# Optimization experiments

Hardware: AMD Instinct MI355X
Metric: run time of the kernel (lower is better)

Reference implementation:

```python
import jax, jax.numpy as jnp
import numpy as np

N_NODES = 100000
N_EDGES = 3200000
IN_CH = 32
HID = 64
OUT_CH = 2


def _sage_conv(x, src, tgt, W_l, W_r, b, n_nodes):
    """PyG SAGEConv with mean aggregation: out = lin_l(mean_agg) + lin_r(x).
    edge (src -> tgt): messages from src nodes are averaged at tgt nodes."""
    msgs = x[src]  # [E, C] gather
    agg = jax.ops.segment_sum(msgs, tgt, num_segments=n_nodes)  # [N, C]
    deg = jax.ops.segment_sum(jnp.ones((src.shape[0],), x.dtype), tgt,
                              num_segments=n_nodes)  # [N]
    agg = agg / jnp.maximum(deg, 1.0)[:, None]
    return agg @ W_l + b + x @ W_r


def _layernorm(x, gamma, beta, eps=1e-5):
    mu = jnp.mean(x, axis=-1, keepdims=True)
    var = jnp.var(x, axis=-1, keepdims=True)
    return (x - mu) * jax.lax.rsqrt(var + eps) * gamma + beta


def setup_inputs() -> dict:
    key = jax.random.key(0)
    ks = jax.random.split(key, 12)
    x = jax.random.normal(ks[0], (N_NODES, IN_CH), dtype=jnp.float32)
    edge_index = jax.random.randint(ks[1], (2, N_EDGES), 0, N_NODES, dtype=jnp.int64)

    def lin(k, fan_in, fan_out):
        s = 1.0 / np.sqrt(fan_in)
        return jax.random.uniform(k, (fan_in, fan_out), jnp.float32, -s, s)

    return {
        "x": x,
        "edge_index": edge_index,
        "W_l1": lin(ks[2], IN_CH, HID), "W_r1": lin(ks[3], IN_CH, HID),
        "b1": jnp.zeros((HID,), jnp.float32),
        "g1": jnp.ones((HID,), jnp.float32), "be1": jnp.zeros((HID,), jnp.float32),
        "W_l2": lin(ks[4], HID, HID), "W_r2": lin(ks[5], HID, HID),
        "b2": jnp.zeros((HID,), jnp.float32),
        "g2": jnp.ones((HID,), jnp.float32), "be2": jnp.zeros((HID,), jnp.float32),
        "W_l3": lin(ks[6], HID, OUT_CH), "W_r3": lin(ks[7], HID, OUT_CH),
        "b3": jnp.zeros((OUT_CH,), jnp.float32),
    }


def reference(x, edge_index, W_l1, W_r1, b1, g1, be1,
              W_l2, W_r2, b2, g2, be2, W_l3, W_r3, b3):
    src = edge_index[0]
    tgt = edge_index[1]
    n = x.shape[0]
    # layer 1: SAGEConv -> LayerNorm -> ReLU (dropout = identity in eval)
    h = _sage_conv(x, src, tgt, W_l1, W_r1, b1, n)
    h = jax.nn.relu(_layernorm(h, g1, be1))
    # layer 2
    h = _sage_conv(h, src, tgt, W_l2, W_r2, b2, n)
    h = jax.nn.relu(_layernorm(h, g2, be2))
    # layer 3 -> logits [N, OUT_CH]
    logits = _sage_conv(h, src, tgt, W_l3, W_r3, b3, n)
    return logits
```

## Files before the change

kernel.cpp:

```cpp
#include <hip/hip_runtime.h>
#include <hip/hip_fp16.h>

#define N_NODES 100000
#define N_EDGES 3200000
#define NBK 391
#define CAP 9216
#define EPB 8192
#define NBLK_BIN 391


__device__ __forceinline__ int wave_incl_scan_i(int v) {
  int lane = threadIdx.x & 63;
#pragma unroll
  for (int off = 1; off < 64; off <<= 1) {
    int n = __shfl_up(v, off);
    if (lane >= off) v += n;
  }
  return v;
}

__device__ __forceinline__ float bcastf(float v, int l) {
  return __int_as_float(__builtin_amdgcn_readlane(__float_as_int(v), l));
}

__device__ __forceinline__ __half2 h2zero() { return __float2half2_rn(0.0f); }

__device__ __forceinline__ __half2 h2shfl_xor_add(__half2 a, int off) {
  int ai = *reinterpret_cast<int*>(&a);
  int bi = __shfl_xor(ai, off);
  return __hadd2(a, *reinterpret_cast<__half2*>(&bi));
}


__global__ __launch_bounds__(256) void init_cursor(int* __restrict__ cursor) {
  int i = blockIdx.x * 256 + threadIdx.x;
  if (i < NBK) cursor[i] = i * CAP;
}

__global__ __launch_bounds__(256) void bin_scatter(const int* __restrict__ src,
                                                   const int* __restrict__ tgt,
                                                   int* __restrict__ cursor,
                                                   unsigned int* __restrict__ binned) {
  __shared__ int hist[NBK];
  __shared__ int lbase[NBK];
  int t = threadIdx.x;
  for (int i = t; i < NBK; i += 256) hist[i] = 0;
  __syncthreads();
  int e0 = blockIdx.x * EPB;
  int e1 = min(e0 + EPB, N_EDGES);
  for (int e = e0 + t; e < e1; e += 256) atomicAdd(&hist[tgt[e] >> 8], 1);
  __syncthreads();
  for (int i = t; i < NBK; i += 256) {
    int c = hist[i];
    lbase[i] = c ? atomicAdd(&cursor[i], c) : 0;
    hist[i] = 0;
  }
  __syncthreads();
  for (int e = e0 + t; e < e1; e += 256) {
    int tg = tgt[e];
    int bkt = tg >> 8;
    int lo = atomicAdd(&hist[bkt], 1);
    binned[lbase[bkt] + lo] = (unsigned int)src[e] | ((unsigned int)(tg & 255) << 17);
  }
}

__global__ __launch_bounds__(256) void bucket_sort(const unsigned int* __restrict__ binned,
                                                   const int* __restrict__ cursor,
                                                   int* __restrict__ csr,
                                                   int* __restrict__ offs) {
  __shared__ int deg[256];
  __shared__ int lcur[256];
  __shared__ int wsum[4];
  int b = blockIdx.x;
  int t = threadIdx.x;
  int base = b * CAP;
  int cnt = cursor[b] - base;
  deg[t] = 0;
  __syncthreads();
  for (int i = t; i < cnt; i += 256) atomicAdd(&deg[binned[base + i] >> 17], 1);
  __syncthreads();
  int v = deg[t];
  int inc = wave_incl_scan_i(v);
  int lane = t & 63, wid = t >> 6;
  if (lane == 63) wsum[wid] = inc;
  __syncthreads();
  if (t == 0) {
    int run = 0;
#pragma unroll
    for (int i = 0; i < 4; i++) { int c = wsum[i]; wsum[i] = run; run += c; }
  }
  __syncthreads();
  int incl = inc + wsum[wid];
  lcur[t] = base + incl - v;
  int node = b * 256 + t;
  if (node < N_NODES) offs[node] = base + incl;
  __syncthreads();
  for (int i = t; i < cnt; i += 256) {
    unsigned int pv = binned[base + i];
    int pos = atomicAdd(&lcur[pv >> 17], 1);
    csr[pos] = (int)(pv & 0x1FFFFu);
  }
}


__global__ __launch_bounds__(256) void to_half2(const float* __restrict__ in,
                                                __half2* __restrict__ out, int n2) {
  int i = blockIdx.x * 256 + threadIdx.x;
  if (i >= n2) return;
  float2 v = reinterpret_cast<const float2*>(in)[i];
  out[i] = __floats2half2_rn(v.x, v.y);
}


__global__ __launch_bounds__(256) void layer1_fused(
    const __half2* __restrict__ xh, const int* __restrict__ csr,
    const int* __restrict__ offs, const float* __restrict__ Wl,
    const float* __restrict__ Wr, const float* __restrict__ b,
    const float* __restrict__ g, const float* __restrict__ be,
    __half* __restrict__ h1) {
  int node = blockIdx.x * 4 + (threadIdx.x >> 6);
  if (node >= N_NODES) return;
  int lane = threadIdx.x & 63;
  int c = lane & 15, slot4 = lane >> 4;

  int end = offs[node];
  int start = (node & 255) ? offs[node - 1] : (node >> 8) * CAP;
  float inv = 1.0f / fmaxf((float)(end - start), 1.0f);

  __half2 A0 = h2zero(), A1 = h2zero(), A2 = h2zero(), A3 = h2zero();
  int slot = start + slot4;
  for (; slot + 12 < end; slot += 16) {
    int s0 = csr[slot], s1 = csr[slot + 4], s2 = csr[slot + 8], s3 = csr[slot + 12];
    A0 = __hadd2(A0, xh[(size_t)s0 * 16 + c]);
    A1 = __hadd2(A1, xh[(size_t)s1 * 16 + c]);
    A2 = __hadd2(A2, xh[(size_t)s2 * 16 + c]);
    A3 = __hadd2(A3, xh[(size_t)s3 * 16 + c]);
  }
  if (slot < end) {
    int i1 = slot + 4, i2 = slot + 8;
    int s0 = csr[slot];
    int s1 = (i1 < end) ? csr[i1] : s0;
    int s2 = (i2 < end) ? csr[i2] : s0;
    __half2 u0 = xh[(size_t)s0 * 16 + c];
    __half2 u1 = xh[(size_t)s1 * 16 + c];
    __half2 u2 = xh[(size_t)s2 * 16 + c];
    A0 = __hadd2(A0, u0);
    A1 = __hadd2(A1, (i1 < end) ? u1 : h2zero());
    A2 = __hadd2(A2, (i2 < end) ? u2 : h2zero());
  }
  __half2 Ah = __hadd2(__hadd2(A0, A1), __hadd2(A2, A3));
  Ah = h2shfl_xor_add(Ah, 16);
  Ah = h2shfl_xor_add(Ah, 32);
  float2 fa = __half22float2(Ah);
  float ax = fa.x * inv, ay = fa.y * inv;

  float2 xs = __half22float2(xh[(size_t)node * 16 + c]);

  int o = lane;
  float accO = b[o];
#pragma unroll
  for (int k = 0; k < 32; k++) {
    float ak = bcastf((k & 1) ? ay : ax, k >> 1);
    float xk = bcastf((k & 1) ? xs.y : xs.x, k >> 1);
    accO = fmaf(ak, Wl[k * 64 + o], accO);
    accO = fmaf(xk, Wr[k * 64 + o], accO);
  }

  float s = accO;
#pragma unroll
  for (int off = 32; off; off >>= 1) s += __shfl_xor(s, off);
  float mu = s * (1.0f / 64.0f);
  float d = accO - mu;
  float v2 = d * d;
#pragma unroll
  for (int off = 32; off; off >>= 1) v2 += __shfl_xor(v2, off);
  float o2 = d * rsqrtf(v2 * (1.0f / 64.0f) + 1e-5f) * g[o] + be[o];
  h1[(size_t)node * 64 + o] = __float2half(fmaxf(o2, 0.0f));
}

__global__ __launch_bounds__(256) void layer2_fused(
    const __half2* __restrict__ h1q, const int* __restrict__ csr,
    const int* __restrict__ offs, const float* __restrict__ Wl,
    const float* __restrict__ Wr, const float* __restrict__ b,
    const float* __restrict__ g, const float* __restrict__ be,
    const float* __restrict__ Wl3, const float* __restrict__ Wr3,
    const float* __restrict__ b3, float* __restrict__ y3,
    float* __restrict__ out) {
  int node = blockIdx.x * 4 + (threadIdx.x >> 6);
  if (node >= N_NODES) return;
  int lane = threadIdx.x & 63;
  int c = lane & 31, half = lane >> 5;

  int end = offs[node];
  int start = (node & 255) ? offs[node - 1] : (node >> 8) * CAP;
  float inv = 1.0f / fmaxf((float)(end - start), 1.0f);

  __half2 A0 = h2zero(), A1 = h2zero(), A2 = h2zero(), A3 = h2zero();
  int slot = start + half;
  for (; slot + 6 < end; slot += 8) {
    int s0 = csr[slot], s1 = csr[slot + 2], s2 = csr[slot + 4], s3 = csr[slot + 6];
    A0 = __hadd2(A0, h1q[(size_t)s0 * 32 + c]);
    A1 = __hadd2(A1, h1q[(size_t)s1 * 32 + c]);
    A2 = __hadd2(A2, h1q[(size_t)s2 * 32 + c]);
    A3 = __hadd2(A3, h1q[(size_t)s3 * 32 + c]);
  }
  if (slot < end) {
    int i1 = slot + 2, i2 = slot + 4;
    int s0 = csr[slot];
    int s1 = (i1 < end) ? csr[i1] : s0;
    int s2 = (i2 < end) ? csr[i2] : s0;
    __half2 u0 = h1q[(size_t)s0 * 32 + c];
    __half2 u1 = h1q[(size_t)s1 * 32 + c];
    __half2 u2 = h1q[(size_t)s2 * 32 + c];
    A0 = __hadd2(A0, u0);
    A1 = __hadd2(A1, (i1 < end) ? u1 : h2zero());
    A2 = __hadd2(A2, (i2 < end) ? u2 : h2zero());
  }
  __half2 Ah = __hadd2(__hadd2(A0, A1), __hadd2(A2, A3));
  Ah = h2shfl_xor_add(Ah, 32);
  float2 fa = __half22float2(Ah);
  float ax = fa.x * inv, ay = fa.y * inv;

  float2 hs = __half22float2(h1q[(size_t)node * 32 + c]);

  int o = lane;
  float accO = b[o];
#pragma unroll
  for (int k = 0; k < 64; k++) {
    float ak = bcastf((k & 1) ? ay : ax, k >> 1);
    float hk = bcastf((k & 1) ? hs.y : hs.x, k >> 1);
    accO = fmaf(ak, Wl[k * 64 + o], accO);
    accO = fmaf(hk, Wr[k * 64 + o], accO);
  }

  float s = accO;
#pragma unroll
  for (int off = 32; off; off >>= 1) s += __shfl_xor(s, off);
  float mu = s * (1.0f / 64.0f);
  float d = accO - mu;
  float v2 = d * d;
#pragma unroll
  for (int off = 32; off; off >>= 1) v2 += __shfl_xor(v2, off);
  float h2v = fmaxf(d * rsqrtf(v2 * (1.0f / 64.0f) + 1e-5f) * g[o] + be[o], 0.0f);

  float t0 = h2v * Wl3[o * 2 + 0];
  float t1 = h2v * Wl3[o * 2 + 1];
  float t2 = h2v * Wr3[o * 2 + 0];
  float t3 = h2v * Wr3[o * 2 + 1];
#pragma unroll
  for (int off = 32; off; off >>= 1) {
    t0 += __shfl_xor(t0, off);
    t1 += __shfl_xor(t1, off);
    t2 += __shfl_xor(t2, off);
    t3 += __shfl_xor(t3, off);
  }
  if (lane == 0) {
    reinterpret_cast<float2*>(y3)[node] = make_float2(t0, t1);
    reinterpret_cast<float2*>(out)[node] = make_float2(t2 + b3[0], t3 + b3[1]);
  }
}

__global__ __launch_bounds__(256) void gather3(
    const float* __restrict__ y, const int* __restrict__ csr,
    const int* __restrict__ offs, float* __restrict__ out) {
  int node = blockIdx.x * 4 + (threadIdx.x >> 6);
  if (node >= N_NODES) return;
  int lane = threadIdx.x & 63;

  int end = offs[node];
  int start = (node & 255) ? offs[node - 1] : (node >> 8) * CAP;
  float inv = 1.0f / fmaxf((float)(end - start), 1.0f);

  float s0 = 0.f, s1 = 0.f;
  for (int slot = start + lane; slot < end; slot += 64) {
    float2 v = reinterpret_cast<const float2*>(y)[csr[slot]];
    s0 += v.x;
    s1 += v.y;
  }
#pragma unroll
  for (int off = 32; off; off >>= 1) {
    s0 += __shfl_xor(s0, off);
    s1 += __shfl_xor(s1, off);
  }
  if (lane == 0) {
    out[(size_t)node * 2 + 0] += s0 * inv;
    out[(size_t)node * 2 + 1] += s1 * inv;
  }
}


extern "C" void kernel_launch(void* const* d_in, const int* in_sizes, int n_in,
                              void* d_out, int out_size, void* d_ws, size_t ws_size,
                              hipStream_t stream) {
  const float* x = (const float*)d_in[0];
  const int* ei = (const int*)d_in[1];
  const int* src = ei;
  const int* tgt = ei + N_EDGES;
  const float* Wl1 = (const float*)d_in[2];
  const float* Wr1 = (const float*)d_in[3];
  const float* b1 = (const float*)d_in[4];
  const float* g1 = (const float*)d_in[5];
  const float* be1 = (const float*)d_in[6];
  const float* Wl2 = (const float*)d_in[7];
  const float* Wr2 = (const float*)d_in[8];
  const float* b2 = (const float*)d_in[9];
  const float* g2 = (const float*)d_in[10];
  const float* be2 = (const float*)d_in[11];
  const float* Wl3 = (const float*)d_in[12];
  const float* Wr3 = (const float*)d_in[13];
  const float* b3 = (const float*)d_in[14];
  float* out = (float*)d_out;
  char* ws = (char*)d_ws;

  size_t p = 0;
  auto carve = [&](size_t bytes) {
    size_t r = p;
    p += (bytes + 255) & ~(size_t)255;
    return r;
  };
  size_t cursor_off = carve((size_t)NBK * 4);
  size_t offs_off = carve((size_t)N_NODES * 4);
  size_t csr_off = carve((size_t)NBK * CAP * 4);
  size_t bin_off = carve((size_t)NBK * CAP * 4);
  size_t h1_off = carve((size_t)N_NODES * 64 * 2);

  int* cursor = (int*)(ws + cursor_off);
  int* offs = (int*)(ws + offs_off);
  int* csr = (int*)(ws + csr_off);
  unsigned int* binned = (unsigned int*)(ws + bin_off);
  __half2* xh = (__half2*)(ws + bin_off);
  float* y3 = (float*)(ws + bin_off + (size_t)N_NODES * 32 * 2);
  __half* h1 = (__half*)(ws + h1_off);

  init_cursor<<<(NBK + 255) / 256, 256, 0, stream>>>(cursor);
  bin_scatter<<<NBLK_BIN, 256, 0, stream>>>(src, tgt, cursor, binned);
  bucket_sort<<<NBK, 256, 0, stream>>>(binned, cursor, csr, offs);

  to_half2<<<(N_NODES * 16 + 255) / 256, 256, 0, stream>>>(x, xh, N_NODES * 16);

  layer1_fused<<<(N_NODES + 3) / 4, 256, 0, stream>>>(
      xh, csr, offs, Wl1, Wr1, b1, g1, be1, h1);

  layer2_fused<<<(N_NODES + 3) / 4, 256, 0, stream>>>(
      (const __half2*)h1, csr, offs, Wl2, Wr2, b2, g2, be2, Wl3, Wr3, b3, y3, out);

  gather3<<<(N_NODES + 3) / 4, 256, 0, stream>>>(y3, csr, offs, out);
}
```

Before: 327.8 us.

## Quantize layer-1 features to FP8 for gather and unroll layer-2 gather deeper

Layer-1 neighbour gathers now read x stored as FP8 (32 bytes per node instead of 64), decoding to fp32 accumulators, with the self term read directly from the fp32 input. The lane layout changes to 8 lanes per node row and 8 edges per step. Separately, layer 2's gather loop is unrolled to 8 independent accumulators to raise memory-level parallelism. The goal is less gather traffic and more loads in flight; FP8 quantization of the input loses precision and may push the error past tolerance.

```diff
diff --git a/kernel.cpp b/kernel.cpp
--- a/kernel.cpp
+++ b/kernel.cpp
@@ -7,6 +7,8 @@
 #define CAP 9216
 #define EPB 8192
 #define NBLK_BIN 391
+
+typedef float v2f __attribute__((ext_vector_type(2)));
 
 
 __device__ __forceinline__ int wave_incl_scan_i(int v) {
@@ -103,65 +105,86 @@
 }
 
 
-__global__ __launch_bounds__(256) void to_half2(const float* __restrict__ in,
-                                                __half2* __restrict__ out, int n2) {
+__global__ __launch_bounds__(256) void to_fp8(const float* __restrict__ x,
+                                              unsigned int* __restrict__ xq, int n) {
   int i = blockIdx.x * 256 + threadIdx.x;
-  if (i >= n2) return;
-  float2 v = reinterpret_cast<const float2*>(in)[i];
-  out[i] = __floats2half2_rn(v.x, v.y);
+  if (i >= n) return;
+  float4 v = reinterpret_cast<const float4*>(x)[i];
+  int w = 0;
+  w = __builtin_amdgcn_cvt_pk_fp8_f32(v.x, v.y, w, false);
+  w = __builtin_amdgcn_cvt_pk_fp8_f32(v.z, v.w, w, true);
+  xq[i] = (unsigned int)w;
 }
 
 
 __global__ __launch_bounds__(256) void layer1_fused(
-    const __half2* __restrict__ xh, const int* __restrict__ csr,
-    const int* __restrict__ offs, const float* __restrict__ Wl,
-    const float* __restrict__ Wr, const float* __restrict__ b,
-    const float* __restrict__ g, const float* __restrict__ be,
-    __half* __restrict__ h1) {
+    const unsigned int* __restrict__ xq, const float* __restrict__ xf,
+    const int* __restrict__ csr, const int* __restrict__ offs,
+    const float* __restrict__ Wl, const float* __restrict__ Wr,
+    const float* __restrict__ b, const float* __restrict__ g,
+    const float* __restrict__ be, __half* __restrict__ h1) {
   int node = blockIdx.x * 4 + (threadIdx.x >> 6);
   if (node >= N_NODES) return;
   int lane = threadIdx.x & 63;
-  int c = lane & 15, slot4 = lane >> 4;
+  int c8 = lane & 7, e8 = lane >> 3;
 
   int end = offs[node];
   int start = (node & 255) ? offs[node - 1] : (node >> 8) * CAP;
   float inv = 1.0f / fmaxf((float)(end - start), 1.0f);
 
-  __half2 A0 = h2zero(), A1 = h2zero(), A2 = h2zero(), A3 = h2zero();
-  int slot = start + slot4;
-  for (; slot + 12 < end; slot += 16) {
-    int s0 = csr[slot], s1 = csr[slot + 4], s2 = csr[slot + 8], s3 = csr[slot + 12];
-    A0 = __hadd2(A0, xh[(size_t)s0 * 16 + c]);
-    A1 = __hadd2(A1, xh[(size_t)s1 * 16 + c]);
-    A2 = __hadd2(A2, xh[(size_t)s2 * 16 + c]);
-    A3 = __hadd2(A3, xh[(size_t)s3 * 16 + c]);
+  v2f a01 = {0.f, 0.f}, a23 = {0.f, 0.f};
+  int slot = start + e8;
+  for (; slot + 24 < end; slot += 32) {
+    unsigned int u0 = xq[(size_t)csr[slot] * 8 + c8];
+    unsigned int u1 = xq[(size_t)csr[slot + 8] * 8 + c8];
+    unsigned int u2 = xq[(size_t)csr[slot + 16] * 8 + c8];
+    unsigned int u3 = xq[(size_t)csr[slot + 24] * 8 + c8];
+    a01 += __builtin_amdgcn_cvt_pk_f32_fp8(u0, false);
+    a23 += __builtin_amdgcn_cvt_pk_f32_fp8(u0, true);
+    a01 += __builtin_amdgcn_cvt_pk_f32_fp8(u1, false);
+    a23 += __builtin_amdgcn_cvt_pk_f32_fp8(u1, true);
+    a01 += __builtin_amdgcn_cvt_pk_f32_fp8(u2, false);
+    a23 += __builtin_amdgcn_cvt_pk_f32_fp8(u2, true);
+    a01 += __builtin_amdgcn_cvt_pk_f32_fp8(u3, false);
+    a23 += __builtin_amdgcn_cvt_pk_f32_fp8(u3, true);
   }
   if (slot < end) {
-    int i1 = slot + 4, i2 = slot + 8;
+    int i1 = slot + 8, i2 = slot + 16;
     int s0 = csr[slot];
     int s1 = (i1 < end) ? csr[i1] : s0;
     int s2 = (i2 < end) ? csr[i2] : s0;
-    __half2 u0 = xh[(size_t)s0 * 16 + c];
-    __half2 u1 = xh[(size_t)s1 * 16 + c];
-    __half2 u2 = xh[(size_t)s2 * 16 + c];
-    A0 = __hadd2(A0, u0);
-    A1 = __hadd2(A1, (i1 < end) ? u1 : h2zero());
-    A2 = __hadd2(A2, (i2 < end) ? u2 : h2zero());
-  }
-  __half2 Ah = __hadd2(__hadd2(A0, A1), __hadd2(A2, A3));
-  Ah = h2shfl_xor_add(Ah, 16);
-  Ah = h2shfl_xor_add(Ah, 32);
-  float2 fa = __half22float2(Ah);
-  float ax = fa.x * inv, ay = fa.y * inv;
-
-  float2 xs = __half22float2(xh[(size_t)node * 16 + c]);
+    unsigned int u0 = xq[(size_t)s0 * 8 + c8];
+    unsigned int u1 = xq[(size_t)s1 * 8 + c8];
+    unsigned int u2 = xq[(size_t)s2 * 8 + c8];
+    float m1 = (i1 < end) ? 1.0f : 0.0f;
+    float m2 = (i2 < end) ? 1.0f : 0.0f;
+    a01 += __builtin_amdgcn_cvt_pk_f32_fp8(u0, false);
+    a23 += __builtin_amdgcn_cvt_pk_f32_fp8(u0, true);
+    a01 += m1 * __builtin_amdgcn_cvt_pk_f32_fp8(u1, false);
+    a23 += m1 * __builtin_amdgcn_cvt_pk_f32_fp8(u1, true);
+    a01 += m2 * __builtin_amdgcn_cvt_pk_f32_fp8(u2, false);
+    a23 += m2 * __builtin_amdgcn_cvt_pk_f32_fp8(u2, true);
+  }
+#pragma unroll
+  for (int off = 8; off < 64; off <<= 1) {
+    a01.x += __shfl_xor(a01.x, off);
+    a01.y += __shfl_xor(a01.y, off);
+    a23.x += __shfl_xor(a23.x, off);
+    a23.y += __shfl_xor(a23.y, off);
+  }
+  a01 *= inv;
+  a23 *= inv;
+
+  float xv = xf[(size_t)node * 32 + (lane & 31)];
 
   int o = lane;
   float accO = b[o];
 #pragma unroll
   for (int k = 0; k < 32; k++) {
-    float ak = bcastf((k & 1) ? ay : ax, k >> 1);
-    float xk = bcastf((k & 1) ? xs.y : xs.x, k >> 1);
+    const int j = k & 3;
+    float ak = bcastf(j == 0 ? a01.x : j == 1 ? a01.y : j == 2 ? a23.x : a23.y,
+                      k >> 2);
+    float xk = bcastf(xv, k);
     accO = fmaf(ak, Wl[k * 64 + o], accO);
     accO = fmaf(xk, Wr[k * 64 + o], accO);
   }
@@ -196,13 +219,27 @@
   float inv = 1.0f / fmaxf((float)(end - start), 1.0f);
 
   __half2 A0 = h2zero(), A1 = h2zero(), A2 = h2zero(), A3 = h2zero();
+  __half2 A4 = h2zero(), A5 = h2zero(), A6 = h2zero(), A7 = h2zero();
   int slot = start + half;
-  for (; slot + 6 < end; slot += 8) {
+  for (; slot + 14 < end; slot += 16) {
+    int s0 = csr[slot], s1 = csr[slot + 2], s2 = csr[slot + 4], s3 = csr[slot + 6];
+    int s4 = csr[slot + 8], s5 = csr[slot + 10], s6 = csr[slot + 12], s7 = csr[slot + 14];
+    A0 = __hadd2(A0, h1q[(size_t)s0 * 32 + c]);
+    A1 = __hadd2(A1, h1q[(size_t)s1 * 32 + c]);
+    A2 = __hadd2(A2, h1q[(size_t)s2 * 32 + c]);
+    A3 = __hadd2(A3, h1q[(size_t)s3 * 32 + c]);
+    A4 = __hadd2(A4, h1q[(size_t)s4 * 32 + c]);
+    A5 = __hadd2(A5, h1q[(size_t)s5 * 32 + c]);
+    A6 = __hadd2(A6, h1q[(size_t)s6 * 32 + c]);
+    A7 = __hadd2(A7, h1q[(size_t)s7 * 32 + c]);
+  }
+  if (slot + 6 < end) {
     int s0 = csr[slot], s1 = csr[slot + 2], s2 = csr[slot + 4], s3 = csr[slot + 6];
     A0 = __hadd2(A0, h1q[(size_t)s0 * 32 + c]);
     A1 = __hadd2(A1, h1q[(size_t)s1 * 32 + c]);
     A2 = __hadd2(A2, h1q[(size_t)s2 * 32 + c]);
     A3 = __hadd2(A3, h1q[(size_t)s3 * 32 + c]);
+    slot += 8;
   }
   if (slot < end) {
     int i1 = slot + 2, i2 = slot + 4;
@@ -212,11 +249,12 @@
     __half2 u0 = h1q[(size_t)s0 * 32 + c];
     __half2 u1 = h1q[(size_t)s1 * 32 + c];
     __half2 u2 = h1q[(size_t)s2 * 32 + c];
-    A0 = __hadd2(A0, u0);
-    A1 = __hadd2(A1, (i1 < end) ? u1 : h2zero());
-    A2 = __hadd2(A2, (i2 < end) ? u2 : h2zero());
-  }
-  __half2 Ah = __hadd2(__hadd2(A0, A1), __hadd2(A2, A3));
+    A4 = __hadd2(A4, u0);
+    A5 = __hadd2(A5, (i1 < end) ? u1 : h2zero());
+    A6 = __hadd2(A6, (i2 < end) ? u2 : h2zero());
+  }
+  __half2 Ah = __hadd2(__hadd2(__hadd2(A0, A1), __hadd2(A2, A3)),
+                       __hadd2(__hadd2(A4, A5), __hadd2(A6, A7)));
   Ah = h2shfl_xor_add(Ah, 32);
   float2 fa = __half22float2(Ah);
   float ax = fa.x * inv, ay = fa.y * inv;
@@ -328,18 +366,18 @@
   int* offs = (int*)(ws + offs_off);
   int* csr = (int*)(ws + csr_off);
   unsigned int* binned = (unsigned int*)(ws + bin_off);
-  __half2* xh = (__half2*)(ws + bin_off);
-  float* y3 = (float*)(ws + bin_off + (size_t)N_NODES * 32 * 2);
+  unsigned int* xq = (unsigned int*)(ws + bin_off);
+  float* y3 = (float*)(ws + bin_off + (size_t)N_NODES * 32);
   __half* h1 = (__half*)(ws + h1_off);
 
   init_cursor<<<(NBK + 255) / 256, 256, 0, stream>>>(cursor);
   bin_scatter<<<NBLK_BIN, 256, 0, stream>>>(src, tgt, cursor, binned);
   bucket_sort<<<NBK, 256, 0, stream>>>(binned, cursor, csr, offs);
 
-  to_half2<<<(N_NODES * 16 + 255) / 256, 256, 0, stream>>>(x, xh, N_NODES * 16);
+  to_fp8<<<(N_NODES * 8 + 255) / 256, 256, 0, stream>>>(x, xq, N_NODES * 8);
 
   layer1_fused<<<(N_NODES + 3) / 4, 256, 0, stream>>>(
-      xh, csr, offs, Wl1, Wr1, b1, g1, be1, h1);
+      xq, x, csr, offs, Wl1, Wr1, b1, g1, be1, h1);
 
   layer2_fused<<<(N_NODES + 3) / 4, 256, 0, stream>>>(
       (const __half2*)h1, csr, offs, Wl2, Wr2, b2, g2, be2, Wl3, Wr3, b3, y3, out);
```

Measured after the change: 309.4 us. 5.6% less time.
